# Kernel tuning notes

Hardware: AMD Instinct MI355X
Metric: run time of the kernel (lower is better)

Reference implementation:

```python
import jax, jax.numpy as jnp
import numpy as np

N_EXPERTS = 8
FDIM1 = 1024
FDIM2 = 512
NUM_CLASSES = 64
BATCH = 16384


def setup_inputs() -> dict:
    key = jax.random.key(0)
    k1, k2, k3, k4, k5, k6 = jax.random.split(key, 6)
    s1 = 1.0 / np.sqrt(FDIM1)
    s2 = 1.0 / np.sqrt(FDIM2)
    return {
        "domain": jax.random.randint(k1, (BATCH,), 0, N_EXPERTS, dtype=jnp.int64 if jax.config.jax_enable_x64 else jnp.int32),
        "x": jax.random.normal(k2, (BATCH, FDIM1), dtype=jnp.float32),
        "W1": jax.random.uniform(k3, (N_EXPERTS, FDIM1, FDIM2), jnp.float32, -s1, s1),
        "b1": jax.random.uniform(k4, (N_EXPERTS, FDIM2), jnp.float32, -s1, s1),
        "W2": jax.random.uniform(k5, (N_EXPERTS, FDIM2, NUM_CLASSES), jnp.float32, -s2, s2),
        "b2": jax.random.uniform(k6, (N_EXPERTS, NUM_CLASSES), jnp.float32, -s2, s2),
    }


def reference(domain, x, W1, b1, W2, b2):
    # All-expert 2-layer MLP (matches torch loop-over-experts + stack):
    # h: [B, E, fdim2]
    h = jax.nn.relu(jnp.einsum("bf,efh->beh", x, W1) + b1[None, :, :])
    # logits: [B, E, C]
    logits = jnp.einsum("beh,ehc->bec", h, W2) + b2[None, :, :]
    # Gather the expert selected by each sample's domain, then softmax.
    sel = jnp.take_along_axis(logits, domain[:, None, None].astype(jnp.int32), axis=1)[:, 0, :]
    return jax.nn.softmax(sel, axis=-1)
```

## Files before the change

kernel.cpp:

```cpp
#include <hip/hip_runtime.h>
#include <hip/hip_bf16.h>

#define BATCH 16384
#define F1    1024
#define F2    512
#define NCLS  64
#define NEXP  8
#define BPAD  (BATCH + NEXP*128)
#define NBM   136
#define NBG1  544
#define NBG2  272

typedef __attribute__((ext_vector_type(8))) short short8;
typedef __attribute__((ext_vector_type(4))) float float4v;

#define O_META   0
#define O_BEXP   4096
#define O_ORDER  8192
#define O_XPH    131072
#define O_XPL    (O_XPH + 35651584)
#define O_W1H    (O_XPL + 35651584)
#define O_W1L    (O_W1H + 8388608)
#define O_W2H    (O_W1L + 8388608)
#define O_W2L    (O_W2H + 524288)
#define O_HH     (O_W2L + 524288)
#define O_HL     (O_HH + 17825792)

__device__ inline short bf16_rn(float f) {
    unsigned u = __builtin_bit_cast(unsigned, f);
    u = (u + 0x7fffu + ((u >> 16) & 1u)) >> 16;
    return (short)u;
}
__device__ inline float bf16_up(short h) {
    return __builtin_bit_cast(float, ((unsigned)(unsigned short)h) << 16);
}
__device__ inline void split2(float v, short& hi, short& lo) {
    hi = bf16_rn(v);
    lo = bf16_rn(v - bf16_up(hi));
}
__device__ inline float4v mfma16(short8 a, short8 b, float4v c) {
    return __builtin_amdgcn_mfma_f32_16x16x32_bf16(a, b, c, 0, 0, 0);
}
__device__ inline void glds16(const void* g, void* l) {
    __builtin_amdgcn_global_load_lds((const __attribute__((address_space(1))) void*)g,
                                     (__attribute__((address_space(3))) void*)l,
                                     16, 0, 0);
}

__global__ void dael_init(const int* __restrict__ domain, int* meta, int* order) {
    __shared__ int hc[NEXP];
    const int b = blockIdx.x, t = threadIdx.x;
    const int i = b * 256 + t;
    if (i < BPAD) order[i] = -1;
    if (b < 64) {
        if (t < NEXP) hc[t] = 0;
        __syncthreads();
        atomicAdd(&hc[domain[i]], 1);
        __syncthreads();
        if (t < NEXP) meta[64 + b * NEXP + t] = hc[t];
    }
}

__global__ void dael_plan(int* meta, int* bexp) {
    __shared__ int cnt[NEXP], soff[NEXP + 1];
    const int t = threadIdx.x;
    if (t < NEXP) {
        int s = 0;
        for (int b = 0; b < 64; ++b) s += meta[64 + b * NEXP + t];
        cnt[t] = s;
    }
    __syncthreads();
    if (t == 0) {
        int acc = 0;
        for (int e = 0; e < NEXP; ++e) {
            soff[e] = acc;
            meta[16 + e] = acc * 128;
            meta[8 + e] = 0;
            acc += (cnt[e] + 127) >> 7;
        }
        soff[NEXP] = acc;
    }
    __syncthreads();
    for (int i = t; i < NBM; i += 256) {
        int ee = -1;
        #pragma unroll
        for (int e = 0; e < NEXP; ++e)
            if (i >= soff[e] && i < soff[e + 1]) ee = e;
        bexp[i] = ee;
    }
}

__global__ void dael_scatter(const int* __restrict__ domain, int* meta, int* order) {
    __shared__ int lc[NEXP], lb[NEXP];
    const int t = threadIdx.x;
    const int i = blockIdx.x * 256 + t;
    if (t < NEXP) lc[t] = 0;
    __syncthreads();
    const int d = domain[i];
    const int r = atomicAdd(&lc[d], 1);
    __syncthreads();
    if (t < NEXP && lc[t] > 0) lb[t] = atomicAdd(&meta[8 + t], lc[t]);
    __syncthreads();
    order[meta[16 + d] + lb[d] + r] = i;
}

#define NPX 1088
#define NPW1 1024
#define NPW2 64
__global__ __launch_bounds__(256)
void dael_pack(const int* __restrict__ order,
               const float* __restrict__ x, short* xph, short* xpl,
               const float* __restrict__ W1, short* w1h, short* w1l,
               const float* __restrict__ W2, short* w2h, short* w2l) {
    const int b = blockIdx.x, t = threadIdx.x;
    if (b < NPX) {
        const int mb = b >> 3, kg = b & 7;
        const int r = t & 127;
        const int samp = order[mb * 128 + r];
        #pragma unroll
        for (int kl = 0; kl < 4; ++kl) {
            const int ks = kg * 4 + kl;
            const size_t tb = (size_t)(mb * 32 + ks) * 4096;
            #pragma unroll
            for (int sl = 0; sl < 2; ++sl) {
                const int s = t + sl * 256;
                const int q = s >> 7;
                short8 vh = {}, vl = {};
                if (samp >= 0) {
                    const float* src = x + (size_t)samp * F1 + ks * 32 + q * 8;
                    float4 f0 = *(const float4*)src;
                    float4 f1 = *(const float4*)(src + 4);
                    float va[8] = {f0.x, f0.y, f0.z, f0.w, f1.x, f1.y, f1.z, f1.w};
                    #pragma unroll
                    for (int i = 0; i < 8; ++i) { short h, l; split2(va[i], h, l); vh[i] = h; vl[i] = l; }
                }
                *(short8*)(xph + tb + s * 8) = vh;
                *(short8*)(xpl + tb + s * 8) = vl;
            }
        }
    } else if (b < NPX + NPW1) {
        const int b2 = b - NPX;
        const int e = b2 >> 7, strip = (b2 >> 5) & 3, ks = b2 & 31;
        const size_t tb = (size_t)((e * 4 + strip) * 32 + ks) * 4096;
        #pragma unroll
        for (int sl = 0; sl < 2; ++sl) {
            const int s = t + sl * 256;
            const int q = s >> 7, r = s & 127;
            const int n = strip * 128 + r;
            short8 vh, vl;
            #pragma unroll
            for (int jj = 0; jj < 8; ++jj) {
                const int k = ks * 32 + q * 8 + jj;
                float v = W1[((size_t)(e * F1 + k)) * F2 + n];
                short h, l; split2(v, h, l); vh[jj] = h; vl[jj] = l;
            }
            *(short8*)(w1h + tb + s * 8) = vh;
            *(short8*)(w1l + tb + s * 8) = vl;
        }
    } else {
        const int b3 = b - NPX - NPW1;
        const int e = b3 >> 3, ks = b3 & 7;
        const size_t tb = (size_t)(e * 8 + ks) * 4096;
        #pragma unroll
        for (int sl = 0; sl < 2; ++sl) {
            const int s = t + sl * 256;
            const int q = s >> 6, c = s & 63;
            short8 vh, vl;
            #pragma unroll
            for (int jj = 0; jj < 8; ++jj) {
                const int k = ks * 64 + q * 8 + jj;
                float v = W2[((size_t)(e * F2 + k)) * NCLS + c];
                short h, l; split2(v, h, l); vh[jj] = h; vl[jj] = l;
            }
            *(short8*)(w2h + tb + s * 8) = vh;
            *(short8*)(w2l + tb + s * 8) = vl;
        }
    }
}

__global__ __launch_bounds__(256, 3)
void dael_gemm1(const int* __restrict__ bexp,
                const short* __restrict__ xph, const short* __restrict__ xpl,
                const short* __restrict__ w1h, const short* __restrict__ w1l,
                const float* __restrict__ b1,
                short* __restrict__ hh, short* __restrict__ hl) {
    const int L = blockIdx.x;
    const int xcd = L & 7, j = L >> 3;
    const int mb = xcd * 17 + (j % 17);
    const int strip = j / 17;
    const int e = bexp[mb];
    if (e < 0) return;
    const int tid = threadIdx.x;
    const int lane = tid & 63, wv = tid >> 6;
    const int quad = lane >> 4, lrow = lane & 15;
    const int r0w = wv * 32;

    __shared__ __align__(16) char SMc[36864];

    const size_t abase = (size_t)(mb * 32) * 4096 + (size_t)(quad * 128 + r0w + lrow) * 8;
    const short* AH = xph + abase;
    const short* AL = xpl + abase;
    const short* Bh = w1h + (size_t)((e * 4 + strip) * 32) * 4096 + tid * 8;
    const short* Bl = w1l + (size_t)((e * 4 + strip) * 32) * 4096 + tid * 8;
    const int d0 = tid * 16;

    float4v acc[2][8] = {};
    int offb[8];
    #pragma unroll
    for (int jj = 0; jj < 8; ++jj) offb[jj] = quad * 2048 + (jj * 16 + lrow) * 16;

    short8 a0h[2], a0l[2], a1h[2], a1l[2];

    #pragma unroll
    for (int i = 0; i < 2; ++i) {
        a0h[i] = *(const short8*)(AH + i * 128);
        a0l[i] = *(const short8*)(AL + i * 128);
    }
    asm volatile("" ::: "memory");
    glds16(Bh,        SMc + d0);
    glds16(Bh + 2048, SMc + 4096 + d0);
    glds16(Bl,        SMc + 8192 + d0);
    glds16(Bl + 2048, SMc + 12288 + d0);
    asm volatile("" ::: "memory");
    #pragma unroll
    for (int i = 0; i < 2; ++i) {
        a1h[i] = *(const short8*)(AH + 4096 + i * 128);
        a1l[i] = *(const short8*)(AL + 4096 + i * 128);
    }

#define G1_ITER(KS, CURH, CURL, DB, DN)                                        \
    {                                                                          \
        if ((KS) == 31) { asm volatile("s_waitcnt vmcnt(0)" ::: "memory"); }   \
        else            { asm volatile("s_waitcnt vmcnt(4)" ::: "memory"); }   \
        __builtin_amdgcn_s_barrier();                                          \
        asm volatile("" ::: "memory");                                         \
        if ((KS) + 1 < 32) {                                                   \
            const int so_ = ((KS) + 1) * 4096;                                 \
            glds16(Bh + so_,        SMc + (DN) + d0);                          \
            glds16(Bh + so_ + 2048, SMc + (DN) + 4096 + d0);                   \
            glds16(Bl + so_,        SMc + (DN) + 8192 + d0);                   \
            glds16(Bl + so_ + 2048, SMc + (DN) + 12288 + d0);                  \
        }                                                                      \
        asm volatile("" ::: "memory");                                         \
        __builtin_amdgcn_s_setprio(1);                                         \
        _Pragma("unroll")                                                      \
        for (int jj = 0; jj < 8; ++jj) {                                       \
            short8 bh = *(const short8*)(SMc + (DB) + offb[jj]);               \
            short8 bl = *(const short8*)(SMc + (DB) + 8192 + offb[jj]);        \
            _Pragma("unroll")                                                  \
            for (int i = 0; i < 2; ++i) {                                      \
                acc[i][jj] = mfma16(CURH[i], bh, acc[i][jj]);                  \
                acc[i][jj] = mfma16(CURH[i], bl, acc[i][jj]);                  \
                acc[i][jj] = mfma16(CURL[i], bh, acc[i][jj]);                  \
            }                                                                  \
        }                                                                      \
        __builtin_amdgcn_s_setprio(0);                                         \
        asm volatile("" ::: "memory");                                         \
        if ((KS) + 2 < 32) {                                                   \
            const int sa_ = ((KS) + 2) * 4096;                                 \
            _Pragma("unroll")                                                  \
            for (int i = 0; i < 2; ++i) {                                      \
                CURH[i] = *(const short8*)(AH + sa_ + i * 128);                \
                CURL[i] = *(const short8*)(AL + sa_ + i * 128);                \
            }                                                                  \
        }                                                                      \
    }

    for (int kb = 0; kb < 32; kb += 2) {
        G1_ITER(kb,     a0h, a0l, 0,     16384);
        G1_ITER(kb + 1, a1h, a1l, 16384, 0);
    }
#undef G1_ITER

    float bv[8];
    #pragma unroll
    for (int jj = 0; jj < 8; ++jj)
        bv[jj] = b1[e * F2 + strip * 128 + jj * 16 + lrow];
    short* T = (short*)SMc;
    #pragma unroll
    for (int plane = 0; plane < 2; ++plane) {
        __syncthreads();
        #pragma unroll
        for (int i = 0; i < 2; ++i)
            #pragma unroll
            for (int jj = 0; jj < 8; ++jj)
                #pragma unroll
                for (int r = 0; r < 4; ++r) {
                    const int m = r0w + i * 16 + quad * 4 + r;
                    const int n = jj * 16 + lrow;
                    float hv = fmaxf(acc[i][jj][r] + bv[jj], 0.f);
                    short hi = bf16_rn(hv);
                    T[m * 136 + n] = plane ? bf16_rn(hv - bf16_up(hi)) : hi;
                }
        __syncthreads();
        short* dst = plane ? hl : hh;
        #pragma unroll
        for (int u = 0; u < 8; ++u) {
            const int sidx = tid + 256 * u;
            const int g = sidx >> 6, m64 = sidx & 63;
            const int mloc = g >> 4, ksl = (g >> 3) & 1, q = g & 7;
            const int m = mloc * 64 + m64;
            const int n = ksl * 64 + q * 8;
            const size_t off = ((size_t)((mb * 2 + mloc) * 8 + strip * 2 + ksl)) * 4096
                               + q * 512 + m64 * 8;
            *(short8*)(dst + off) = *(const short8*)&T[m * 136 + n];
        }
    }
}

__global__ __launch_bounds__(256)
void dael_gemm2(const int* __restrict__ order, const int* __restrict__ bexp,
                const short* __restrict__ hh, const short* __restrict__ hl,
                const short* __restrict__ w2h, const short* __restrict__ w2l,
                const float* __restrict__ b2, float* __restrict__ out) {
    const int b = blockIdx.x;
    const int e = bexp[b >> 1];
    if (e < 0) return;
    const int p0 = b * 64;
    const int tid = threadIdx.x;
    const int lane = tid & 63, wv = tid >> 6;
    const int quad = lane >> 4, lrow = lane & 15;

    __shared__ __align__(16) char SM2[65536];
    __shared__ float inv[64];

    const short* Ah = hh + (size_t)(b * 8) * 4096 + tid * 8;
    const short* Al = hl + (size_t)(b * 8) * 4096 + tid * 8;
    const short* Bh = w2h + (size_t)(e * 8) * 4096 + tid * 8;
    const short* Bl = w2l + (size_t)(e * 8) * 4096 + tid * 8;
    const int d0 = tid * 16;

    float4v acc[4] = {};

    {
        glds16(Ah,        SM2 + d0);
        glds16(Ah + 2048, SM2 + 4096 + d0);
        glds16(Al,        SM2 + 8192 + d0);
        glds16(Al + 2048, SM2 + 12288 + d0);
        glds16(Bh,        SM2 + 16384 + d0);
        glds16(Bh + 2048, SM2 + 20480 + d0);
        glds16(Bl,        SM2 + 24576 + d0);
        glds16(Bl + 2048, SM2 + 28672 + d0);
    }

    for (int ks = 0; ks < 8; ++ks) {
        __syncthreads();
        if (ks + 1 < 8) {
            const int so = (ks + 1) * 4096;
            const int db = ((ks + 1) & 1) * 32768;
            glds16(Ah + so,        SM2 + db + d0);
            glds16(Ah + so + 2048, SM2 + db + 4096 + d0);
            glds16(Al + so,        SM2 + db + 8192 + d0);
            glds16(Al + so + 2048, SM2 + db + 12288 + d0);
            glds16(Bh + so,        SM2 + db + 16384 + d0);
            glds16(Bh + so + 2048, SM2 + db + 20480 + d0);
            glds16(Bl + so,        SM2 + db + 24576 + d0);
            glds16(Bl + so + 2048, SM2 + db + 28672 + d0);
        }
        const int db = (ks & 1) * 32768;
        #pragma unroll
        for (int ksub = 0; ksub < 2; ++ksub) {
            const int qa = (ksub * 4 + quad) * 1024;
            const int ao = db + qa + (wv * 16 + lrow) * 16;
            short8 ahf = *(const short8*)(SM2 + ao);
            short8 alf = *(const short8*)(SM2 + 8192 + ao);
            #pragma unroll
            for (int jj = 0; jj < 4; ++jj) {
                const int bo = db + 16384 + qa + (jj * 16 + lrow) * 16;
                short8 bh = *(const short8*)(SM2 + bo);
                short8 bl = *(const short8*)(SM2 + 8192 + bo);
                acc[jj] = mfma16(ahf, bh, acc[jj]);
                acc[jj] = mfma16(ahf, bl, acc[jj]);
                acc[jj] = mfma16(alf, bh, acc[jj]);
            }
        }
    }

    __syncthreads();
    float* Lx = (float*)SM2;
    #pragma unroll
    for (int jj = 0; jj < 4; ++jj) {
        const int n = jj * 16 + lrow;
        const float bb = b2[e * NCLS + n];
        #pragma unroll
        for (int r = 0; r < 4; ++r)
            Lx[(wv * 16 + quad * 4 + r) * 68 + n] = acc[jj][r] + bb;
    }
    __syncthreads();
    if (tid < 64) {
        float mx = -3.402823466e38f;
        #pragma unroll 8
        for (int c = 0; c < NCLS; ++c) mx = fmaxf(mx, Lx[tid * 68 + c]);
        float s = 0.f;
        #pragma unroll 8
        for (int c = 0; c < NCLS; ++c) {
            float ev = __expf(Lx[tid * 68 + c] - mx);
            Lx[tid * 68 + c] = ev; s += ev;
        }
        inv[tid] = 1.f / s;
    }
    __syncthreads();
    const int r = tid >> 2, cs = (tid & 3) * 16;
    const int samp = order[p0 + r];
    if (samp >= 0) {
        const float sc = inv[r];
        #pragma unroll
        for (int q = 0; q < 4; ++q) {
            float4 v = *(const float4*)&Lx[r * 68 + cs + q * 4];
            v.x *= sc; v.y *= sc; v.z *= sc; v.w *= sc;
            *(float4*)(out + (size_t)samp * NCLS + cs + q * 4) = v;
        }
    }
}

extern "C" void kernel_launch(void* const* d_in, const int* in_sizes, int n_in,
                              void* d_out, int out_size, void* d_ws, size_t ws_size,
                              hipStream_t stream) {
    const int*   domain = (const int*)d_in[0];
    const float* x      = (const float*)d_in[1];
    const float* W1     = (const float*)d_in[2];
    const float* b1     = (const float*)d_in[3];
    const float* W2     = (const float*)d_in[4];
    const float* b2     = (const float*)d_in[5];
    float* out = (float*)d_out;

    char* ws = (char*)d_ws;
    int*   meta  = (int*)(ws + O_META);
    int*   bexp  = (int*)(ws + O_BEXP);
    int*   order = (int*)(ws + O_ORDER);
    short* xph   = (short*)(ws + O_XPH);
    short* xpl   = (short*)(ws + O_XPL);
    short* w1h   = (short*)(ws + O_W1H);
    short* w1l   = (short*)(ws + O_W1L);
    short* w2h   = (short*)(ws + O_W2H);
    short* w2l   = (short*)(ws + O_W2L);
    short* hh    = (short*)(ws + O_HH);
    short* hl    = (short*)(ws + O_HL);

    dael_init<<<68, 256, 0, stream>>>(domain, meta, order);
    dael_plan<<<1, 256, 0, stream>>>(meta, bexp);
    dael_scatter<<<64, 256, 0, stream>>>(domain, meta, order);
    dael_pack<<<NPX + NPW1 + NPW2, 256, 0, stream>>>(order, x, xph, xpl,
                                                     W1, w1h, w1l, W2, w2h, w2l);
    dael_gemm1<<<NBG1, 256, 0, stream>>>(bexp, xph, xpl, w1h, w1l, b1, hh, hl);
    dael_gemm2<<<NBG2, 256, 0, stream>>>(order, bexp, hh, hl, w2h, w2l, b2, out);
}
```

Measured before the change: 222.9 us.

## Fuse x gather and bf16 split into gemm1, drop packed x buffers

Removes the separate pass that gathered x rows by expert order and wrote hi/lo bf16 planes. gemm1 now loads fp32 x rows directly through the order index and splits them into hi/lo bf16 in registers with packed conversions. The W1/W2 packing is merged into the init kernel, which saves a launch. The B-tile LDS pipeline goes from two to three buffers. Each x element is now re-read and re-split by all four strip blocks, and more LDS per block may lower occupancy.

```diff
diff --git a/kernel.cpp b/kernel.cpp
--- a/kernel.cpp
+++ b/kernel.cpp
@@ -46,101 +46,48 @@
                                      (__attribute__((address_space(3))) void*)l,
                                      16, 0, 0);
 }
-
-__global__ void dael_init(const int* __restrict__ domain, int* meta, int* order) {
+__device__ inline unsigned cvt_pk_bf16(float a, float b) {
+    __hip_bfloat162 h = __float22bfloat162_rn(make_float2(a, b));
+    union { __hip_bfloat162 v; unsigned u; } cv;
+    cv.v = h;
+    return cv.u;
+}
+__device__ inline void splitA8(const float4& r0, const float4& r1, short8& vh, short8& vl) {
+    float f[8] = {r0.x, r0.y, r0.z, r0.w, r1.x, r1.y, r1.z, r1.w};
+    #pragma unroll
+    for (int p = 0; p < 4; ++p) {
+        unsigned hu = cvt_pk_bf16(f[2*p], f[2*p+1]);
+        vh[2*p]   = (short)(hu & 0xFFFFu);
+        vh[2*p+1] = (short)(hu >> 16);
+        float fh0 = __builtin_bit_cast(float, hu << 16);
+        float fh1 = __builtin_bit_cast(float, hu & 0xFFFF0000u);
+        unsigned lu = cvt_pk_bf16(f[2*p] - fh0, f[2*p+1] - fh1);
+        vl[2*p]   = (short)(lu & 0xFFFFu);
+        vl[2*p+1] = (short)(lu >> 16);
+    }
+}
+
+#define NPW1 1024
+#define NPW2 64
+__global__ __launch_bounds__(256)
+void dael_init_pack(const int* __restrict__ domain, int* meta, int* order,
+                    const float* __restrict__ W1, short* w1h, short* w1l,
+                    const float* __restrict__ W2, short* w2h, short* w2l) {
     __shared__ int hc[NEXP];
     const int b = blockIdx.x, t = threadIdx.x;
-    const int i = b * 256 + t;
-    if (i < BPAD) order[i] = -1;
+    if (b < 68) {
+        const int i = b * 256 + t;
+        if (i < BPAD) order[i] = -1;
+    }
     if (b < 64) {
         if (t < NEXP) hc[t] = 0;
         __syncthreads();
-        atomicAdd(&hc[domain[i]], 1);
+        atomicAdd(&hc[domain[b * 256 + t]], 1);
         __syncthreads();
         if (t < NEXP) meta[64 + b * NEXP + t] = hc[t];
     }
-}
-
-__global__ void dael_plan(int* meta, int* bexp) {
-    __shared__ int cnt[NEXP], soff[NEXP + 1];
-    const int t = threadIdx.x;
-    if (t < NEXP) {
-        int s = 0;
-        for (int b = 0; b < 64; ++b) s += meta[64 + b * NEXP + t];
-        cnt[t] = s;
-    }
-    __syncthreads();
-    if (t == 0) {
-        int acc = 0;
-        for (int e = 0; e < NEXP; ++e) {
-            soff[e] = acc;
-            meta[16 + e] = acc * 128;
-            meta[8 + e] = 0;
-            acc += (cnt[e] + 127) >> 7;
-        }
-        soff[NEXP] = acc;
-    }
-    __syncthreads();
-    for (int i = t; i < NBM; i += 256) {
-        int ee = -1;
-        #pragma unroll
-        for (int e = 0; e < NEXP; ++e)
-            if (i >= soff[e] && i < soff[e + 1]) ee = e;
-        bexp[i] = ee;
-    }
-}
-
-__global__ void dael_scatter(const int* __restrict__ domain, int* meta, int* order) {
-    __shared__ int lc[NEXP], lb[NEXP];
-    const int t = threadIdx.x;
-    const int i = blockIdx.x * 256 + t;
-    if (t < NEXP) lc[t] = 0;
-    __syncthreads();
-    const int d = domain[i];
-    const int r = atomicAdd(&lc[d], 1);
-    __syncthreads();
-    if (t < NEXP && lc[t] > 0) lb[t] = atomicAdd(&meta[8 + t], lc[t]);
-    __syncthreads();
-    order[meta[16 + d] + lb[d] + r] = i;
-}
-
-#define NPX 1088
-#define NPW1 1024
-#define NPW2 64
-__global__ __launch_bounds__(256)
-void dael_pack(const int* __restrict__ order,
-               const float* __restrict__ x, short* xph, short* xpl,
-               const float* __restrict__ W1, short* w1h, short* w1l,
-               const float* __restrict__ W2, short* w2h, short* w2l) {
-    const int b = blockIdx.x, t = threadIdx.x;
-    if (b < NPX) {
-        const int mb = b >> 3, kg = b & 7;
-        const int r = t & 127;
-        const int samp = order[mb * 128 + r];
-        #pragma unroll
-        for (int kl = 0; kl < 4; ++kl) {
-            const int ks = kg * 4 + kl;
-            const size_t tb = (size_t)(mb * 32 + ks) * 4096;
-            #pragma unroll
-            for (int sl = 0; sl < 2; ++sl) {
-                const int s = t + sl * 256;
-                const int q = s >> 7;
-                short8 vh = {}, vl = {};
-                if (samp >= 0) {
-                    const float* src = x + (size_t)samp * F1 + ks * 32 + q * 8;
-                    float4 f0 = *(const float4*)src;
-                    float4 f1 = *(const float4*)(src + 4);
-                    float va[8] = {f0.x, f0.y, f0.z, f0.w, f1.x, f1.y, f1.z, f1.w};
-                    #pragma unroll
-                    for (int i = 0; i < 8; ++i) { short h, l; split2(va[i], h, l); vh[i] = h; vl[i] = l; }
-                }
-                *(short8*)(xph + tb + s * 8) = vh;
-                *(short8*)(xpl + tb + s * 8) = vl;
-            }
-        }
-    } else if (b < NPX + NPW1) {
-        const int b2 = b - NPX;
-        const int e = b2 >> 7, strip = (b2 >> 5) & 3, ks = b2 & 31;
+    if (b < NPW1) {
+        const int e = b >> 7, strip = (b >> 5) & 3, ks = b & 31;
         const size_t tb = (size_t)((e * 4 + strip) * 32 + ks) * 4096;
         #pragma unroll
         for (int sl = 0; sl < 2; ++sl) {
@@ -158,7 +105,7 @@
             *(short8*)(w1l + tb + s * 8) = vl;
         }
     } else {
-        const int b3 = b - NPX - NPW1;
+        const int b3 = b - NPW1;
         const int e = b3 >> 3, ks = b3 & 7;
         const size_t tb = (size_t)(e * 8 + ks) * 4096;
         #pragma unroll
@@ -178,9 +125,52 @@
     }
 }
 
+__global__ void dael_plan(int* meta, int* bexp) {
+    __shared__ int cnt[NEXP], soff[NEXP + 1];
+    const int t = threadIdx.x;
+    if (t < NEXP) {
+        int s = 0;
+        for (int b = 0; b < 64; ++b) s += meta[64 + b * NEXP + t];
+        cnt[t] = s;
+    }
+    __syncthreads();
+    if (t == 0) {
+        int acc = 0;
+        for (int e = 0; e < NEXP; ++e) {
+            soff[e] = acc;
+            meta[16 + e] = acc * 128;
+            meta[8 + e] = 0;
+            acc += (cnt[e] + 127) >> 7;
+        }
+        soff[NEXP] = acc;
+    }
+    __syncthreads();
+    for (int i = t; i < NBM; i += 256) {
+        int ee = -1;
+        #pragma unroll
+        for (int e = 0; e < NEXP; ++e)
+            if (i >= soff[e] && i < soff[e + 1]) ee = e;
+        bexp[i] = ee;
+    }
+}
+
+__global__ void dael_scatter(const int* __restrict__ domain, int* meta, int* order) {
+    __shared__ int lc[NEXP], lb[NEXP];
+    const int t = threadIdx.x;
+    const int i = blockIdx.x * 256 + t;
+    if (t < NEXP) lc[t] = 0;
+    __syncthreads();
+    const int d = domain[i];
+    const int r = atomicAdd(&lc[d], 1);
+    __syncthreads();
+    if (t < NEXP && lc[t] > 0) lb[t] = atomicAdd(&meta[8 + t], lc[t]);
+    __syncthreads();
+    order[meta[16 + d] + lb[d] + r] = i;
+}
+
 __global__ __launch_bounds__(256, 3)
-void dael_gemm1(const int* __restrict__ bexp,
-                const short* __restrict__ xph, const short* __restrict__ xpl,
+void dael_gemm1(const int* __restrict__ order, const int* __restrict__ bexp,
+                const float* __restrict__ x,
                 const short* __restrict__ w1h, const short* __restrict__ w1l,
                 const float* __restrict__ b1,
                 short* __restrict__ hh, short* __restrict__ hl) {
@@ -195,11 +185,14 @@
     const int quad = lane >> 4, lrow = lane & 15;
     const int r0w = wv * 32;
 
-    __shared__ __align__(16) char SMc[36864];
-
-    const size_t abase = (size_t)(mb * 32) * 4096 + (size_t)(quad * 128 + r0w + lrow) * 8;
-    const short* AH = xph + abase;
-    const short* AL = xpl + abase;
+    __shared__ __align__(16) char SMc[49152];
+
+    int s0 = order[mb * 128 + r0w + lrow];
+    int s1 = order[mb * 128 + r0w + 16 + lrow];
+    if (s0 < 0) s0 = 0;
+    if (s1 < 0) s1 = 0;
+    const float* xb0 = x + (size_t)s0 * F1 + quad * 8;
+    const float* xb1 = x + (size_t)s1 * F1 + quad * 8;
     const short* Bh = w1h + (size_t)((e * 4 + strip) * 32) * 4096 + tid * 8;
     const short* Bl = w1l + (size_t)((e * 4 + strip) * 32) * 4096 + tid * 8;
     const int d0 = tid * 16;
@@ -209,66 +202,73 @@
     #pragma unroll
     for (int jj = 0; jj < 8; ++jj) offb[jj] = quad * 2048 + (jj * 16 + lrow) * 16;
 
-    short8 a0h[2], a0l[2], a1h[2], a1l[2];
-
-    #pragma unroll
-    for (int i = 0; i < 2; ++i) {
-        a0h[i] = *(const short8*)(AH + i * 128);
-        a0l[i] = *(const short8*)(AL + i * 128);
-    }
-    asm volatile("" ::: "memory");
+    float4 ra0[4], ra1[4];
+    int c0 = 0, c1 = 16384, c2 = 32768;
+
     glds16(Bh,        SMc + d0);
     glds16(Bh + 2048, SMc + 4096 + d0);
     glds16(Bl,        SMc + 8192 + d0);
     glds16(Bl + 2048, SMc + 12288 + d0);
     asm volatile("" ::: "memory");
-    #pragma unroll
-    for (int i = 0; i < 2; ++i) {
-        a1h[i] = *(const short8*)(AH + 4096 + i * 128);
-        a1l[i] = *(const short8*)(AL + 4096 + i * 128);
-    }
-
-#define G1_ITER(KS, CURH, CURL, DB, DN)                                        \
+    ra0[0] = *(const float4*)(xb0);
+    ra0[1] = *(const float4*)(xb0 + 4);
+    ra0[2] = *(const float4*)(xb1);
+    ra0[3] = *(const float4*)(xb1 + 4);
+    asm volatile("" ::: "memory");
+    glds16(Bh + 4096,        SMc + 16384 + d0);
+    glds16(Bh + 4096 + 2048, SMc + 16384 + 4096 + d0);
+    glds16(Bl + 4096,        SMc + 16384 + 8192 + d0);
+    glds16(Bl + 4096 + 2048, SMc + 16384 + 12288 + d0);
+    asm volatile("" ::: "memory");
+    ra1[0] = *(const float4*)(xb0 + 32);
+    ra1[1] = *(const float4*)(xb0 + 36);
+    ra1[2] = *(const float4*)(xb1 + 32);
+    ra1[3] = *(const float4*)(xb1 + 36);
+
+#define G1_ITER(KS, RA)                                                        \
     {                                                                          \
         if ((KS) == 31) { asm volatile("s_waitcnt vmcnt(0)" ::: "memory"); }   \
-        else            { asm volatile("s_waitcnt vmcnt(4)" ::: "memory"); }   \
+        else            { asm volatile("s_waitcnt vmcnt(8)" ::: "memory"); }   \
         __builtin_amdgcn_s_barrier();                                          \
         asm volatile("" ::: "memory");                                         \
-        if ((KS) + 1 < 32) {                                                   \
-            const int so_ = ((KS) + 1) * 4096;                                 \
-            glds16(Bh + so_,        SMc + (DN) + d0);                          \
-            glds16(Bh + so_ + 2048, SMc + (DN) + 4096 + d0);                   \
-            glds16(Bl + so_,        SMc + (DN) + 8192 + d0);                   \
-            glds16(Bl + so_ + 2048, SMc + (DN) + 12288 + d0);                  \
+        if ((KS) + 2 < 32) {                                                   \
+            const int so_ = ((KS) + 2) * 4096;                                 \
+            glds16(Bh + so_,        SMc + c2 + d0);                            \
+            glds16(Bh + so_ + 2048, SMc + c2 + 4096 + d0);                     \
+            glds16(Bl + so_,        SMc + c2 + 8192 + d0);                     \
+            glds16(Bl + so_ + 2048, SMc + c2 + 12288 + d0);                    \
         }                                                                      \
         asm volatile("" ::: "memory");                                         \
+        short8 ah[2], al[2];                                                   \
+        splitA8(RA[0], RA[1], ah[0], al[0]);                                   \
+        splitA8(RA[2], RA[3], ah[1], al[1]);                                   \
         __builtin_amdgcn_s_setprio(1);                                         \
         _Pragma("unroll")                                                      \
         for (int jj = 0; jj < 8; ++jj) {                                       \
-            short8 bh = *(const short8*)(SMc + (DB) + offb[jj]);               \
-            short8 bl = *(const short8*)(SMc + (DB) + 8192 + offb[jj]);        \
+            short8 bh = *(const short8*)(SMc + c0 + offb[jj]);                 \
+            short8 bl = *(const short8*)(SMc + c0 + 8192 + offb[jj]);          \
             _Pragma("unroll")                                                  \
             for (int i = 0; i < 2; ++i) {                                      \
-                acc[i][jj] = mfma16(CURH[i], bh, acc[i][jj]);                  \
-                acc[i][jj] = mfma16(CURH[i], bl, acc[i][jj]);                  \
-                acc[i][jj] = mfma16(CURL[i], bh, acc[i][jj]);                  \
+                acc[i][jj] = mfma16(ah[i], bh, acc[i][jj]);                    \
+                acc[i][jj] = mfma16(ah[i], bl, acc[i][jj]);                    \
+                acc[i][jj] = mfma16(al[i], bh, acc[i][jj]);                    \
             }                                                                  \
         }                                                                      \
         __builtin_amdgcn_s_setprio(0);                                         \
         asm volatile("" ::: "memory");                                         \
         if ((KS) + 2 < 32) {                                                   \
-            const int sa_ = ((KS) + 2) * 4096;                                 \
-            _Pragma("unroll")                                                  \
-            for (int i = 0; i < 2; ++i) {                                      \
-                CURH[i] = *(const short8*)(AH + sa_ + i * 128);                \
-                CURL[i] = *(const short8*)(AL + sa_ + i * 128);                \
-            }                                                                  \
+            const int ao_ = ((KS) + 2) * 32;                                   \
+            RA[0] = *(const float4*)(xb0 + ao_);                               \
+            RA[1] = *(const float4*)(xb0 + ao_ + 4);                           \
+            RA[2] = *(const float4*)(xb1 + ao_);                               \
+            RA[3] = *(const float4*)(xb1 + ao_ + 4);                           \
         }                                                                      \
+        { const int tmp_ = c0; c0 = c1; c1 = c2; c2 = tmp_; }                  \
     }
 
     for (int kb = 0; kb < 32; kb += 2) {
-        G1_ITER(kb,     a0h, a0l, 0,     16384);
-        G1_ITER(kb + 1, a1h, a1l, 16384, 0);
+        G1_ITER(kb,     ra0);
+        G1_ITER(kb + 1, ra1);
     }
 #undef G1_ITER
 
@@ -428,8 +428,6 @@
     int*   meta  = (int*)(ws + O_META);
     int*   bexp  = (int*)(ws + O_BEXP);
     int*   order = (int*)(ws + O_ORDER);
-    short* xph   = (short*)(ws + O_XPH);
-    short* xpl   = (short*)(ws + O_XPL);
     short* w1h   = (short*)(ws + O_W1H);
     short* w1l   = (short*)(ws + O_W1L);
     short* w2h   = (short*)(ws + O_W2H);
@@ -437,11 +435,10 @@
     short* hh    = (short*)(ws + O_HH);
     short* hl    = (short*)(ws + O_HL);
 
-    dael_init<<<68, 256, 0, stream>>>(domain, meta, order);
+    dael_init_pack<<<NPW1 + NPW2, 256, 0, stream>>>(domain, meta, order,
+                                                    W1, w1h, w1l, W2, w2h, w2l);
     dael_plan<<<1, 256, 0, stream>>>(meta, bexp);
     dael_scatter<<<64, 256, 0, stream>>>(domain, meta, order);
-    dael_pack<<<NPX + NPW1 + NPW2, 256, 0, stream>>>(order, x, xph, xpl,
-                                                     W1, w1h, w1l, W2, w2h, w2l);
-    dael_gemm1<<<NBG1, 256, 0, stream>>>(bexp, xph, xpl, w1h, w1l, b1, hh, hl);
+    dael_gemm1<<<NBG1, 256, 0, stream>>>(order, bexp, x, w1h, w1l, b1, hh, hl);
     dael_gemm2<<<NBG2, 256, 0, stream>>>(order, bexp, hh, hl, w2h, w2l, b2, out);
 }
```

Result: faster. 203.9 us (-8.5%).
